# Kernel optimization log

Hardware: AMD Instinct MI355X
Metric: run time of the kernel (lower is better)

Reference implementation:

```python
import jax, jax.numpy as jnp
import numpy as np

B, T, D = 8, 1024, 768
H, DH = 12, 64
E, K, DFF = 16, 2, 3072
EPS = 1e-5


def _ln(x, w, b):
    m = x.mean(-1, keepdims=True)
    v = ((x - m) ** 2).mean(-1, keepdims=True)
    return (x - m) * jax.lax.rsqrt(v + EPS) * w + b


def setup_inputs() -> dict:
    key = jax.random.key(0)
    ks = jax.random.split(key, 12)
    s = 0.02
    return {
        "x": jax.random.normal(ks[0], (B, T, D), jnp.float32),
        "ln1_w": jnp.ones((D,), jnp.float32),
        "ln1_b": jnp.zeros((D,), jnp.float32),
        "qkv_w": jax.random.normal(ks[1], (D, 3 * D), jnp.float32) * s,
        "qkv_b": jnp.zeros((3 * D,), jnp.float32),
        "proj_w": jax.random.normal(ks[2], (D, D), jnp.float32) * s,
        "proj_b": jnp.zeros((D,), jnp.float32),
        "ln2_w": jnp.ones((D,), jnp.float32),
        "ln2_b": jnp.zeros((D,), jnp.float32),
        "router_w": jax.random.normal(ks[3], (D, E), jnp.float32) * s,
        "w1": jax.random.normal(ks[4], (E, D, DFF), jnp.float32) * s,
        "b1": jnp.zeros((E, DFF), jnp.float32),
        "w2": jax.random.normal(ks[5], (E, DFF, D), jnp.float32) * s,
        "b2": jnp.zeros((E, D), jnp.float32),
    }


def _block(x, ln1_w, ln1_b, qkv_w, qkv_b, proj_w, proj_b,
           ln2_w, ln2_b, router_w, w1, b1, w2, b2):
    # --- attention ---
    h = _ln(x, ln1_w, ln1_b)
    qkv = h @ qkv_w + qkv_b                      # [B,T,3D]
    q, k, v = jnp.split(qkv, 3, axis=-1)
    q = q.reshape(B, T, H, DH).transpose(0, 2, 1, 3)
    k = k.reshape(B, T, H, DH).transpose(0, 2, 1, 3)
    v = v.reshape(B, T, H, DH).transpose(0, 2, 1, 3)
    scores = jnp.einsum("bhqd,bhkd->bhqk", q, k) / np.sqrt(DH)
    causal = jnp.tril(jnp.ones((T, T), bool))
    scores = jnp.where(causal, scores, -jnp.inf)
    attn = jax.nn.softmax(scores, axis=-1)
    y = jnp.einsum("bhqk,bhkd->bhqd", attn, v)
    y = y.transpose(0, 2, 1, 3).reshape(B, T, D)
    x = x + y @ proj_w + proj_b                  # residual 1

    # --- MoE FFN (dense all-experts, gated combine) ---
    z = _ln(x, ln2_w, ln2_b)                     # [B,T,D]
    probs = jax.nn.softmax(z @ router_w, axis=-1)  # [B,T,E]
    top_p, ix = jax.lax.top_k(probs, K)
    gate = (jax.nn.one_hot(ix, E, dtype=probs.dtype) * top_p[..., None]).sum(-2)  # [B,T,E]
    gate_e = jnp.moveaxis(gate, -1, 0)           # [E,B,T]

    def body(acc, ew):
        g, W1, B1, W2, B2 = ew
        out = jax.nn.gelu(z @ W1 + B1, approximate=False) @ W2 + B2
        return acc + g[..., None] * out, None

    yff, _ = jax.lax.scan(body, jnp.zeros_like(z), (gate_e, w1, b1, w2, b2))
    # MoELayer returns z + yff; Block adds x again (faithful double residual)
    return x + z + yff


def reference(x, ln1_w, ln1_b, qkv_w, qkv_b, proj_w, proj_b,
              ln2_w, ln2_b, router_w, w1, b1, w2, b2):
    return _block(x, ln1_w, ln1_b, qkv_w, qkv_b, proj_w, proj_b,
                  ln2_w, ln2_b, router_w, w1, b1, w2, b2)
```

## Files before the change

kernel.cpp:

```cpp
#include <hip/hip_runtime.h>
#include <math.h>

#define D_MODEL 768
#define T_SEQ   1024
#define B_BATCH 8
#define NTOK    8192
#define H_HEADS 12
#define DHEAD   64
#define NEXP    16
#define DFF     3072
#define NPAIR   16384
#define MAXT128 144
#define MAXT256 80

typedef unsigned short u16;
typedef unsigned int   u32;

typedef __attribute__((ext_vector_type(8))) short bf16x8;
typedef __attribute__((ext_vector_type(4))) float f32x4;
typedef __attribute__((ext_vector_type(4))) u32   u32x4;

__device__ __forceinline__ float bf2f(u16 u) { return __uint_as_float(((u32)u) << 16); }
__device__ __forceinline__ u16 f2bf(float f) {
    u32 u = __float_as_uint(f);
    return (u16)((u + 0x7FFFu + ((u >> 16) & 1u)) >> 16);
}

__device__ __forceinline__ float fast_gelu(float v) {
    float u2 = -1.5957691216f * v * (1.0f + 0.044715f * v * v);
    return v / (1.0f + __expf(u2));
}

__device__ __forceinline__ void gload16(const void* g, void* l) {
    __builtin_amdgcn_global_load_lds((const __attribute__((address_space(1))) void*)g,
                                     (__attribute__((address_space(3))) void*)l, 16, 0, 0);
}

__global__ __launch_bounds__(256) void ln_kernel(const float* __restrict__ x,
                                                 const float* __restrict__ w,
                                                 const float* __restrict__ b,
                                                 u16* __restrict__ out_bf,
                                                 float* __restrict__ out_f) {
    const int row = blockIdx.x;
    const int tid = threadIdx.x;
    const float* xr = x + (size_t)row * D_MODEL;
    float v0 = xr[tid], v1 = xr[tid + 256], v2 = xr[tid + 512];
    float s = v0 + v1 + v2;
    float s2 = v0 * v0 + v1 * v1 + v2 * v2;
#pragma unroll
    for (int o = 32; o > 0; o >>= 1) { s += __shfl_down(s, o); s2 += __shfl_down(s2, o); }
    __shared__ float red[8];
    __shared__ float stats[2];
    const int wid = tid >> 6;
    if ((tid & 63) == 0) { red[wid] = s; red[4 + wid] = s2; }
    __syncthreads();
    if (tid == 0) {
        float ts = red[0] + red[1] + red[2] + red[3];
        float ts2 = red[4] + red[5] + red[6] + red[7];
        float mean = ts * (1.0f / D_MODEL);
        float var = ts2 * (1.0f / D_MODEL) - mean * mean;
        stats[0] = mean;
        stats[1] = rsqrtf(var + 1e-5f);
    }
    __syncthreads();
    const float mean = stats[0], rstd = stats[1];
    u16* orow = out_bf + (size_t)row * D_MODEL;
    float r0 = (v0 - mean) * rstd * w[tid]       + b[tid];
    float r1 = (v1 - mean) * rstd * w[tid + 256] + b[tid + 256];
    float r2 = (v2 - mean) * rstd * w[tid + 512] + b[tid + 512];
    orow[tid] = f2bf(r0); orow[tid + 256] = f2bf(r1); orow[tid + 512] = f2bf(r2);
    if (out_f) {
        float* frow = out_f + (size_t)row * D_MODEL;
        frow[tid] = r0; frow[tid + 256] = r1; frow[tid + 512] = r2;
    }
}

__global__ __launch_bounds__(256) void transpose_cvt(const float* __restrict__ src,
                                                     u16* __restrict__ dst,
                                                     int R, int C) {
    const size_t plane = (size_t)R * C;
    src += (size_t)blockIdx.z * plane;
    dst += (size_t)blockIdx.z * plane;
    __shared__ __align__(16) u16 tile[64][72];
    const int t = threadIdx.x;
    const int r0 = blockIdx.y * 64, c0 = blockIdx.x * 64;
    {
        const int lr = t >> 2, lc = (t & 3) * 16;
        const float* sp = src + (size_t)(r0 + lr) * C + c0 + lc;
        u16 tmp[16];
#pragma unroll
        for (int j = 0; j < 4; ++j) {
            f32x4 f = *(const f32x4*)(sp + j * 4);
            tmp[j * 4 + 0] = f2bf(f[0]); tmp[j * 4 + 1] = f2bf(f[1]);
            tmp[j * 4 + 2] = f2bf(f[2]); tmp[j * 4 + 3] = f2bf(f[3]);
        }
        *(u32x4*)&tile[lr][lc]     = *(const u32x4*)&tmp[0];
        *(u32x4*)&tile[lr][lc + 8] = *(const u32x4*)&tmp[8];
    }
    __syncthreads();
    {
        const int ln = t >> 2, lk0 = (t & 3) * 16;
        u16 o[16];
#pragma unroll
        for (int j = 0; j < 16; ++j) o[j] = tile[lk0 + j][ln];
        u16* d = dst + (size_t)(c0 + ln) * R + r0 + lk0;
        *(u32x4*)&d[0] = *(const u32x4*)&o[0];
        *(u32x4*)&d[8] = *(const u32x4*)&o[8];
    }
}

template <int MODE>
__global__ __launch_bounds__(512, 4) void gemm256(
    const u16* __restrict__ A, const u16* __restrict__ Bt,
    const float* __restrict__ bias, void* __restrict__ Cout,
    const float* __restrict__ resid,
    const int* __restrict__ bucket_tok, const int* __restrict__ offsets,
    const int* __restrict__ counts, const int* __restrict__ desc_e,
    const int* __restrict__ desc_r, const int* __restrict__ tile_cnt,
    int K, int N)
{
    const u32 nwg  = gridDim.x * gridDim.y;
    const u32 orig = blockIdx.x + gridDim.x * blockIdx.y;
    const u32 flat = (nwg & 7u) ? orig : ((orig & 7u) * (nwg >> 3) + (orig >> 3));
    const int bx = (int)(flat % gridDim.x);
    const int by = (int)(flat / gridDim.x);

    int e = 0, r0 = 0, off = 0, ne = 0, row0 = 0;
    const int col0 = bx * 128;
    if constexpr (MODE >= 2) {
        if (by >= *tile_cnt) return;
        e = desc_e[by];
        r0 = desc_r[by];
        off = offsets[e];
        ne = counts[e];
    } else {
        row0 = by * 256;
    }
    if constexpr (MODE == 2) Bt += (size_t)e * D_MODEL * DFF;
    if constexpr (MODE == 3) Bt += (size_t)e * DFF * D_MODEL;

    __shared__ __align__(16) u16 AsBs[256 * 64 + 128 * 64];
    u16* As = AsBs;
    u16* Bs = AsBs + 256 * 64;

    const int tid = threadIdx.x;
    const int lane = tid & 63;
    const int w = tid >> 6;
    const int wm = w >> 1, wn = w & 1;
    const int fr = lane & 15, fg = lane >> 4;

    const int koff = ((((tid & 7) * 16) ^ (((tid >> 3) & 7) << 4)) >> 1);

    u32 aoff[4];
#pragma unroll
    for (int i = 0; i < 4; ++i) {
        const int r = i * 64 + (tid >> 3);
        u32 row;
        if constexpr (MODE == 2) {
            int rb = r0 + r;
            row = (u32)bucket_tok[off + (rb < ne ? rb : 0)];
        } else if constexpr (MODE == 3) {
            int rb = r0 + r;
            row = (u32)(off + (rb < ne ? rb : (ne - 1)));
        } else {
            row = (u32)(row0 + r);
        }
        aoff[i] = row * (u32)K + (u32)koff;
    }
    u32 boff[2];
#pragma unroll
    for (int i = 0; i < 2; ++i) {
        const int n = i * 64 + (tid >> 3);
        boff[i] = (u32)(col0 + n) * (u32)K + (u32)koff;
    }

    f32x4 acc[4][4] = {};

    for (int k0 = 0; k0 < K; k0 += 64) {
        __syncthreads();
#pragma unroll
        for (int i = 0; i < 4; ++i)
            gload16(A + aoff[i] + k0, &As[(i * 512 + w * 64) * 8]);
#pragma unroll
        for (int i = 0; i < 2; ++i)
            gload16(Bt + boff[i] + k0, &Bs[(i * 512 + w * 64) * 8]);
        __syncthreads();
#pragma unroll
        for (int kk = 0; kk < 2; ++kk) {
            const int sw = ((kk * 64 + fg * 16) ^ ((fr & 7) << 4)) >> 1;
            bf16x8 a[4], b[4];
#pragma unroll
            for (int mi = 0; mi < 4; ++mi)
                a[mi] = *(const bf16x8*)&As[(wm * 64 + mi * 16 + fr) * 64 + sw];
#pragma unroll
            for (int ni = 0; ni < 4; ++ni)
                b[ni] = *(const bf16x8*)&Bs[(wn * 64 + ni * 16 + fr) * 64 + sw];
#pragma unroll
            for (int mi = 0; mi < 4; ++mi)
#pragma unroll
                for (int ni = 0; ni < 4; ++ni)
                    acc[mi][ni] = __builtin_amdgcn_mfma_f32_16x16x32_bf16(a[mi], b[ni], acc[mi][ni], 0, 0, 0);
        }
    }

    __syncthreads();
    float* slab = (float*)AsBs + w * 1088;
    const int er = lane >> 2;
    const int ec = (lane & 3) * 16;
    const int colb = col0 + wn * 64 + ec;

#pragma unroll
    for (int mi = 0; mi < 4; ++mi) {
#pragma unroll
        for (int ni = 0; ni < 4; ++ni)
#pragma unroll
            for (int i = 0; i < 4; ++i)
                slab[(fg * 4 + i) * 68 + ni * 16 + fr] = acc[mi][ni][i];
        __syncthreads();
        f32x4 v[4];
#pragma unroll
        for (int q = 0; q < 4; ++q) v[q] = *(const f32x4*)&slab[er * 68 + ec + q * 4];
        const int lrow = wm * 64 + mi * 16 + er;

        if constexpr (MODE == 0) {
            u16 o[16];
#pragma unroll
            for (int q = 0; q < 4; ++q) {
                f32x4 b4 = *(const f32x4*)&bias[colb + q * 4];
#pragma unroll
                for (int j = 0; j < 4; ++j) o[q * 4 + j] = f2bf(v[q][j] + b4[j]);
            }
            u16* cp = (u16*)Cout + (size_t)(row0 + lrow) * N + colb;
            *(u32x4*)cp       = *(const u32x4*)&o[0];
            *(u32x4*)(cp + 8) = *(const u32x4*)&o[8];
        } else if constexpr (MODE == 1) {
            float* cp = (float*)Cout + (size_t)(row0 + lrow) * N + colb;
            const float* rp = resid + (size_t)(row0 + lrow) * N + colb;
#pragma unroll
            for (int q = 0; q < 4; ++q) {
                f32x4 b4 = *(const f32x4*)&bias[colb + q * 4];
                f32x4 r4 = *(const f32x4*)(rp + q * 4);
                f32x4 o4;
#pragma unroll
                for (int j = 0; j < 4; ++j) o4[j] = v[q][j] + b4[j] + r4[j];
                *(f32x4*)(cp + q * 4) = o4;
            }
        } else if constexpr (MODE == 2) {
            const int rb = r0 + lrow;
            if (rb < ne) {
                u16 o[16];
#pragma unroll
                for (int q = 0; q < 4; ++q) {
                    f32x4 b4 = *(const f32x4*)&bias[(size_t)e * DFF + colb + q * 4];
#pragma unroll
                    for (int j = 0; j < 4; ++j) o[q * 4 + j] = f2bf(fast_gelu(v[q][j] + b4[j]));
                }
                u16* cp = (u16*)Cout + (size_t)(off + rb) * N + colb;
                *(u32x4*)cp       = *(const u32x4*)&o[0];
                *(u32x4*)(cp + 8) = *(const u32x4*)&o[8];
            }
        } else {
            const int rb = r0 + lrow;
            if (rb < ne) {
                float* cp = (float*)Cout + (size_t)(off + rb) * N + colb;
#pragma unroll
                for (int q = 0; q < 4; ++q) {
                    f32x4 b4 = *(const f32x4*)&bias[(size_t)e * D_MODEL + colb + q * 4];
                    f32x4 o4;
#pragma unroll
                    for (int j = 0; j < 4; ++j) o4[j] = v[q][j] + b4[j];
                    *(f32x4*)(cp + q * 4) = o4;
                }
            }
        }
        if (mi < 3) __syncthreads();
    }
}

template <int MODE>
__global__ __launch_bounds__(256) void gemm128f(
    const u16* __restrict__ A, const float* __restrict__ Bf,
    const float* __restrict__ bias, void* __restrict__ Cout,
    const float* __restrict__ resid,
    const int* __restrict__ bucket_tok, const int* __restrict__ offsets,
    const int* __restrict__ counts, const int* __restrict__ desc_e,
    const int* __restrict__ desc_r, const int* __restrict__ tile_cnt,
    int K, int N)
{
    int e = 0, r0 = 0, off = 0, ne = 0, row0 = 0;
    const int col0 = blockIdx.x * 128;
    if constexpr (MODE >= 2) {
        if ((int)blockIdx.y >= *tile_cnt) return;
        e = desc_e[blockIdx.y]; r0 = desc_r[blockIdx.y];
        off = offsets[e]; ne = counts[e];
    } else row0 = blockIdx.y * 128;
    if constexpr (MODE == 2) Bf += (size_t)e * D_MODEL * DFF;
    if constexpr (MODE == 3) Bf += (size_t)e * DFF * D_MODEL;

    __shared__ __align__(16) u16 AsL[128 * 32];
    __shared__ __align__(16) u16 BsL[128 * 32];

    const int tid = threadIdx.x;
    const int lane = tid & 63;
    const int w = tid >> 6;
    const int wr = (w >> 1) * 64, wc = (w & 1) * 64;
    const int fr = lane & 15, fg = lane >> 4;
    const int lrow = lane >> 2, lk = (lane & 3) * 8;

    const u16* ag[2];
#pragma unroll
    for (int i = 0; i < 2; ++i) {
        int r = i * 64 + w * 16 + lrow;
        size_t srow;
        if constexpr (MODE == 2) {
            int rb = r0 + r;
            int tok = bucket_tok[off + (rb < ne ? rb : 0)];
            srow = (size_t)tok * K;
        } else if constexpr (MODE == 3) {
            int rb = r0 + r;
            int pp = off + (rb < ne ? rb : (ne - 1));
            srow = (size_t)pp * K;
        } else srow = (size_t)(row0 + r) * K;
        ag[i] = A + srow + lk;
    }

    f32x4 acc[4][4] = {};
    for (int k0 = 0; k0 < K; k0 += 32) {
        __syncthreads();
        gload16(ag[0] + k0, &AsL[0 * 2048 + w * 512]);
        gload16(ag[1] + k0, &AsL[1 * 2048 + w * 512]);
#pragma unroll
        for (int i = 0; i < 4; ++i) {
            int s = tid + 256 * i;
            int kk = s >> 5, n4 = (s & 31) * 4;
            f32x4 f = *(const f32x4*)(Bf + (size_t)(k0 + kk) * N + col0 + n4);
            BsL[(n4 + 0) * 32 + kk] = f2bf(f[0]);
            BsL[(n4 + 1) * 32 + kk] = f2bf(f[1]);
            BsL[(n4 + 2) * 32 + kk] = f2bf(f[2]);
            BsL[(n4 + 3) * 32 + kk] = f2bf(f[3]);
        }
        __syncthreads();
        bf16x8 a[4], b[4];
#pragma unroll
        for (int mi = 0; mi < 4; ++mi)
            a[mi] = *(const bf16x8*)&AsL[(wr + mi * 16 + fr) * 32 + fg * 8];
#pragma unroll
        for (int ni = 0; ni < 4; ++ni)
            b[ni] = *(const bf16x8*)&BsL[(wc + ni * 16 + fr) * 32 + fg * 8];
#pragma unroll
        for (int mi = 0; mi < 4; ++mi)
#pragma unroll
            for (int ni = 0; ni < 4; ++ni)
                acc[mi][ni] = __builtin_amdgcn_mfma_f32_16x16x32_bf16(a[mi], b[ni], acc[mi][ni], 0, 0, 0);
    }
#pragma unroll
    for (int mi = 0; mi < 4; ++mi) {
#pragma unroll
        for (int ni = 0; ni < 4; ++ni) {
            const int lr = wr + mi * 16 + fg * 4;
            const int col = col0 + wc + ni * 16 + fr;
#pragma unroll
            for (int i = 0; i < 4; ++i) {
                float v = acc[mi][ni][i];
                if constexpr (MODE == 0) {
                    int grow = row0 + lr + i;
                    ((u16*)Cout)[(size_t)grow * N + col] = f2bf(v + bias[col]);
                } else if constexpr (MODE == 1) {
                    int grow = row0 + lr + i;
                    size_t idx = (size_t)grow * N + col;
                    ((float*)Cout)[idx] = resid[idx] + v + bias[col];
                } else if constexpr (MODE == 2) {
                    int rb = r0 + lr + i;
                    if (rb < ne) {
                        float vb = v + bias[(size_t)e * DFF + col];
                        ((u16*)Cout)[(size_t)(off + rb) * N + col] = f2bf(fast_gelu(vb));
                    }
                } else {
                    int rb = r0 + lr + i;
                    if (rb < ne) {
                        ((float*)Cout)[(size_t)(off + rb) * N + col] = v + bias[(size_t)e * D_MODEL + col];
                    }
                }
            }
        }
    }
}

__global__ __launch_bounds__(256) void attn_mfma(const u16* __restrict__ qkv,
                                                 u16* __restrict__ y) {
    const int bh = blockIdx.x;
    const int b = bh / H_HEADS, h = bh % H_HEADS;
    const int qt = gridDim.y - 1 - blockIdx.y;
    const int tid = threadIdx.x, lane = tid & 63, w = tid >> 6;
    const int fr = lane & 15, fg = lane >> 4;

    __shared__ __align__(16) u16 Ks[64][72];
    __shared__ __align__(16) u16 Vt[64][72];
    __shared__ __align__(16) u16 Ps[4][32][72];

    const int tb = b * T_SEQ + qt * 128;
    const int wrow = w * 32;

    bf16x8 aq[2][2];
#pragma unroll
    for (int rg = 0; rg < 2; ++rg) {
        const u16* qp = qkv + (size_t)(tb + wrow + rg * 16 + fr) * (3 * D_MODEL) + h * DHEAD + fg * 8;
        aq[rg][0] = *(const bf16x8*)qp;
        aq[rg][1] = *(const bf16x8*)(qp + 32);
    }
    f32x4 accO[2][4] = {};
    float m_[2][4], l_[2][4];
#pragma unroll
    for (int rg = 0; rg < 2; ++rg)
#pragma unroll
        for (int i = 0; i < 4; ++i) { m_[rg][i] = -1e30f; l_[rg][i] = 0.0f; }

    const int ktmax = 2 * qt + 1;
    for (int kt = 0; kt <= ktmax; ++kt) {
        __syncthreads();
        {
            const int krow = tid >> 2, c16 = (tid & 3) * 16;
            const u16* kp = qkv + (size_t)(b * T_SEQ + kt * 64 + krow) * (3 * D_MODEL)
                          + D_MODEL + h * DHEAD + c16;
            *(u32x4*)&Ks[krow][c16]     = *(const u32x4*)kp;
            *(u32x4*)&Ks[krow][c16 + 8] = *(const u32x4*)(kp + 8);
            const u16* vp = kp + D_MODEL;
            u16 vv[16];
            *(u32x4*)&vv[0] = *(const u32x4*)vp;
            *(u32x4*)&vv[8] = *(const u32x4*)(vp + 8);
#pragma unroll
            for (int j = 0; j < 16; ++j) Vt[c16 + j][krow] = vv[j];
        }
        __syncthreads();

        if (kt * 64 > qt * 128 + wrow + 31) continue;

#pragma unroll
        for (int rg = 0; rg < 2; ++rg) {
            f32x4 s4[4] = {};
#pragma unroll
            for (int kk = 0; kk < 2; ++kk) {
#pragma unroll
                for (int ni = 0; ni < 4; ++ni) {
                    bf16x8 bk = *(const bf16x8*)&Ks[ni * 16 + fr][kk * 32 + fg * 8];
                    s4[ni] = __builtin_amdgcn_mfma_f32_16x16x32_bf16(aq[rg][kk], bk, s4[ni], 0, 0, 0);
                }
            }
            float p[4][4];
#pragma unroll
            for (int i = 0; i < 4; ++i) {
                const int grow = qt * 128 + wrow + rg * 16 + fg * 4 + i;
                float rmax = -1e30f;
#pragma unroll
                for (int ni = 0; ni < 4; ++ni) {
                    float v = s4[ni][i] * 0.125f;
                    if (kt * 64 + ni * 16 + fr > grow) v = -1e30f;
                    p[ni][i] = v;
                    rmax = fmaxf(rmax, v);
                }
#pragma unroll
                for (int msk = 1; msk < 16; msk <<= 1) rmax = fmaxf(rmax, __shfl_xor(rmax, msk));
                const float mn = fmaxf(m_[rg][i], rmax);
                float sum = 0.0f;
#pragma unroll
                for (int ni = 0; ni < 4; ++ni) {
                    float ev = __expf(p[ni][i] - mn);
                    p[ni][i] = ev;
                    sum += ev;
                }
#pragma unroll
                for (int msk = 1; msk < 16; msk <<= 1) sum += __shfl_xor(sum, msk);
                const float sc = __expf(m_[rg][i] - mn);
                l_[rg][i] = l_[rg][i] * sc + sum;
                m_[rg][i] = mn;
#pragma unroll
                for (int ni = 0; ni < 4; ++ni) accO[rg][ni][i] *= sc;
#pragma unroll
                for (int ni = 0; ni < 4; ++ni)
                    Ps[w][rg * 16 + fg * 4 + i][ni * 16 + fr] = f2bf(p[ni][i]);
            }
        }

#pragma unroll
        for (int rg = 0; rg < 2; ++rg) {
#pragma unroll
            for (int kk = 0; kk < 2; ++kk) {
                bf16x8 ap = *(const bf16x8*)&Ps[w][rg * 16 + fr][kk * 32 + fg * 8];
#pragma unroll
                for (int ni = 0; ni < 4; ++ni) {
                    bf16x8 bv = *(const bf16x8*)&Vt[ni * 16 + fr][kk * 32 + fg * 8];
                    accO[rg][ni] = __builtin_amdgcn_mfma_f32_16x16x32_bf16(ap, bv, accO[rg][ni], 0, 0, 0);
                }
            }
        }
    }

#pragma unroll
    for (int rg = 0; rg < 2; ++rg) {
#pragma unroll
        for (int i = 0; i < 4; ++i) {
            const float inv = 1.0f / l_[rg][i];
            u16* yp = y + (size_t)(tb + wrow + rg * 16 + fg * 4 + i) * D_MODEL + h * DHEAD;
#pragma unroll
            for (int ni = 0; ni < 4; ++ni) yp[ni * 16 + fr] = f2bf(accO[rg][ni][i] * inv);
        }
    }
}

__global__ __launch_bounds__(64) void router_kernel(const float* __restrict__ z,
                                                    const float* __restrict__ rw,
                                                    float* __restrict__ gates,
                                                    int* __restrict__ eidx) {
    const int t = blockIdx.x;
    const int lane = threadIdx.x;
    const int e = lane & 15, part = lane >> 4;
    const float* zr = z + (size_t)t * D_MODEL;
    float acc = 0.0f;
    for (int d = part * 192; d < part * 192 + 192; ++d)
        acc += zr[d] * rw[d * NEXP + e];
    acc += __shfl_down(acc, 32);
    acc += __shfl_down(acc, 16);
    const float lg = acc;
    float logit[NEXP];
#pragma unroll
    for (int ee = 0; ee < NEXP; ++ee) logit[ee] = __shfl(lg, ee);
    if (lane == 0) {
        float m1 = -1e30f, m2 = -1e30f; int i1 = 0, i2 = 0;
#pragma unroll
        for (int ee = 0; ee < NEXP; ++ee) {
            float v = logit[ee];
            if (v > m1) { m2 = m1; i2 = i1; m1 = v; i1 = ee; }
            else if (v > m2) { m2 = v; i2 = ee; }
        }
        float den = 0.0f;
#pragma unroll
        for (int ee = 0; ee < NEXP; ++ee) den += __expf(logit[ee] - m1);
        const float inv = 1.0f / den;
        gates[2 * t] = inv;
        gates[2 * t + 1] = __expf(m2 - m1) * inv;
        eidx[2 * t] = i1;
        eidx[2 * t + 1] = i2;
    }
}

__global__ __launch_bounds__(256) void count_kernel(const int* __restrict__ eidx, int* counts) {
    int i = blockIdx.x * 256 + threadIdx.x;
    if (i < NPAIR) atomicAdd(&counts[eidx[i]], 1);
}

__global__ void offsets_kernel(const int* __restrict__ counts, int* offsets, int* cursor,
                               int* desc_e, int* desc_r, int* tile_cnt, int step) {
    if (threadIdx.x == 0 && blockIdx.x == 0) {
        int off = 0, nt = 0;
        for (int e = 0; e < NEXP; ++e) {
            offsets[e] = off;
            cursor[e] = off;
            int c = counts[e];
            for (int r = 0; r < c; r += step) { desc_e[nt] = e; desc_r[nt] = r; ++nt; }
            off += c;
        }
        *tile_cnt = nt;
    }
}

__global__ __launch_bounds__(256) void scatter_kernel(const int* __restrict__ eidx, int* cursor,
                                                      int* __restrict__ btok, int* __restrict__ ppos) {
    int i = blockIdx.x * 256 + threadIdx.x;
    if (i < NPAIR) {
        int pos = atomicAdd(&cursor[eidx[i]], 1);
        btok[pos] = i >> 1;
        ppos[i] = pos;
    }
}

__global__ __launch_bounds__(256) void final_kernel(const float* __restrict__ x1,
                                                    const float* __restrict__ zf,
                                                    const float* __restrict__ moe_o,
                                                    const float* __restrict__ gates,
                                                    const int* __restrict__ ppos,
                                                    float* __restrict__ out) {
    const int t = blockIdx.x;
    const int d = blockIdx.y * 256 + threadIdx.x;
    const size_t idx = (size_t)t * D_MODEL + d;
    const float g0 = gates[2 * t], g1 = gates[2 * t + 1];
    const int p0 = ppos[2 * t], p1 = ppos[2 * t + 1];
    out[idx] = x1[idx] + zf[idx] + g0 * moe_o[(size_t)p0 * D_MODEL + d]
                                 + g1 * moe_o[(size_t)p1 * D_MODEL + d];
}

extern "C" void kernel_launch(void* const* d_in, const int* in_sizes, int n_in,
                              void* d_out, int out_size, void* d_ws, size_t ws_size,
                              hipStream_t stream) {
    const float* x        = (const float*)d_in[0];
    const float* ln1_w    = (const float*)d_in[1];
    const float* ln1_b    = (const float*)d_in[2];
    const float* qkv_w    = (const float*)d_in[3];
    const float* qkv_b    = (const float*)d_in[4];
    const float* proj_w   = (const float*)d_in[5];
    const float* proj_b   = (const float*)d_in[6];
    const float* ln2_w    = (const float*)d_in[7];
    const float* ln2_b    = (const float*)d_in[8];
    const float* router_w = (const float*)d_in[9];
    const float* w1       = (const float*)d_in[10];
    const float* b1       = (const float*)d_in[11];
    const float* w2       = (const float*)d_in[12];
    const float* b2       = (const float*)d_in[13];
    float* out = (float*)d_out;

    char* ws = (char*)d_ws;
    size_t off = 0;
    auto alloc = [&](size_t bytes) -> void* {
        void* p = ws + off;
        off += (bytes + 255) & ~(size_t)255;
        return p;
    };
    u16*  h_bf   = (u16*)alloc((size_t)NTOK * D_MODEL * 2);
    u16*  qkv_bf = (u16*)alloc((size_t)NTOK * 3 * D_MODEL * 2);
    u16*  y_bf   = h_bf;
    float* x1    = (float*)alloc((size_t)NTOK * D_MODEL * 4);
    u16*  z_bf   = (u16*)alloc((size_t)NTOK * D_MODEL * 2);
    float* z_f   = (float*)alloc((size_t)NTOK * D_MODEL * 4);
    u16*  act    = (u16*)alloc((size_t)NPAIR * DFF * 2);
    float* moe_o = (float*)alloc((size_t)NPAIR * D_MODEL * 4);
    float* gates = (float*)alloc((size_t)NTOK * 2 * 4);
    int*  eidx   = (int*)alloc((size_t)NTOK * 2 * 4);
    int*  ppos   = (int*)alloc((size_t)NTOK * 2 * 4);
    int*  btok   = (int*)alloc((size_t)NPAIR * 4);
    int*  counts = (int*)alloc(NEXP * 4);
    int*  offs   = (int*)alloc(NEXP * 4);
    int*  cursor = (int*)alloc(NEXP * 4);
    int*  desc_e = (int*)alloc(MAXT128 * 4);
    int*  desc_r = (int*)alloc(MAXT128 * 4);
    int*  tcnt   = (int*)alloc(4);
    u16* qkvT  = (u16*)alloc((size_t)(3 * D_MODEL) * D_MODEL * 2);
    u16* projT = (u16*)alloc((size_t)D_MODEL * D_MODEL * 2);
    u16* w1t   = (u16*)alloc((size_t)NEXP * DFF * D_MODEL * 2);
    u16* w2t   = (u16*)alloc((size_t)NEXP * D_MODEL * DFF * 2);
    const bool useT = (off <= ws_size);
    (void)in_sizes; (void)n_in; (void)out_size;

    hipMemsetAsync(counts, 0, NEXP * 4, stream);

    if (useT) {
        transpose_cvt<<<dim3(3 * D_MODEL / 64, D_MODEL / 64, 1), 256, 0, stream>>>(qkv_w, qkvT, D_MODEL, 3 * D_MODEL);
        transpose_cvt<<<dim3(D_MODEL / 64, D_MODEL / 64, 1), 256, 0, stream>>>(proj_w, projT, D_MODEL, D_MODEL);
        transpose_cvt<<<dim3(DFF / 64, D_MODEL / 64, NEXP), 256, 0, stream>>>(w1, w1t, D_MODEL, DFF);
        transpose_cvt<<<dim3(D_MODEL / 64, DFF / 64, NEXP), 256, 0, stream>>>(w2, w2t, DFF, D_MODEL);
    }

    ln_kernel<<<NTOK, 256, 0, stream>>>(x, ln1_w, ln1_b, h_bf, nullptr);
    if (useT)
        gemm256<0><<<dim3(18, 32), 512, 0, stream>>>(h_bf, qkvT, qkv_b, qkv_bf, nullptr,
            nullptr, nullptr, nullptr, nullptr, nullptr, nullptr, D_MODEL, 3 * D_MODEL);
    else
        gemm128f<0><<<dim3(18, 64), 256, 0, stream>>>(h_bf, qkv_w, qkv_b, qkv_bf, nullptr,
            nullptr, nullptr, nullptr, nullptr, nullptr, nullptr, D_MODEL, 3 * D_MODEL);

    attn_mfma<<<dim3(B_BATCH * H_HEADS, T_SEQ / 128), 256, 0, stream>>>(qkv_bf, y_bf);

    if (useT)
        gemm256<1><<<dim3(6, 32), 512, 0, stream>>>(y_bf, projT, proj_b, x1, x,
            nullptr, nullptr, nullptr, nullptr, nullptr, nullptr, D_MODEL, D_MODEL);
    else
        gemm128f<1><<<dim3(6, 64), 256, 0, stream>>>(y_bf, proj_w, proj_b, x1, x,
            nullptr, nullptr, nullptr, nullptr, nullptr, nullptr, D_MODEL, D_MODEL);

    ln_kernel<<<NTOK, 256, 0, stream>>>(x1, ln2_w, ln2_b, z_bf, z_f);
    router_kernel<<<NTOK, 64, 0, stream>>>(z_f, router_w, gates, eidx);
    count_kernel<<<NPAIR / 256, 256, 0, stream>>>(eidx, counts);
    offsets_kernel<<<1, 64, 0, stream>>>(counts, offs, cursor, desc_e, desc_r, tcnt,
                                         useT ? 256 : 128);
    scatter_kernel<<<NPAIR / 256, 256, 0, stream>>>(eidx, cursor, btok, ppos);

    if (useT) {
        gemm256<2><<<dim3(DFF / 128, MAXT256), 512, 0, stream>>>(z_bf, w1t, b1, act, nullptr,
            btok, offs, counts, desc_e, desc_r, tcnt, D_MODEL, DFF);
        gemm256<3><<<dim3(D_MODEL / 128, MAXT256), 512, 0, stream>>>(act, w2t, b2, moe_o, nullptr,
            btok, offs, counts, desc_e, desc_r, tcnt, DFF, D_MODEL);
    } else {
        gemm128f<2><<<dim3(DFF / 128, MAXT128), 256, 0, stream>>>(z_bf, w1, b1, act, nullptr,
            btok, offs, counts, desc_e, desc_r, tcnt, D_MODEL, DFF);
        gemm128f<3><<<dim3(D_MODEL / 128, MAXT128), 256, 0, stream>>>(act, w2, b2, moe_o, nullptr,
            btok, offs, counts, desc_e, desc_r, tcnt, DFF, D_MODEL);
    }

    final_kernel<<<dim3(NTOK, 3), 256, 0, stream>>>(x1, z_f, moe_o, gates, ppos, out);
}
```

Measured before the change: 665.2 us.

## Add double-buffered 256x256-tile GEMM for QKV and MoE expert matmuls

Adds a new GEMM kernel with 256x256 output tiles, with each wave computing a 128x64 sub-tile, and double-buffered LDS so the next K-slice's global loads overlap the current MFMA work. It is used for the QKV projection and both MoE expert GEMMs. The projection GEMM keeps the old single-buffered 256x128 kernel, now specialized to residual mode only. The larger tiles raise data reuse per byte loaded, but use 128 KB of LDS and twice the accumulator registers, which lowers occupancy. They also give fewer workgroups per launch, so the small-N MoE down-projection gets only 3 column tiles.

```diff
diff --git a/kernel.cpp b/kernel.cpp
--- a/kernel.cpp
+++ b/kernel.cpp
@@ -110,10 +110,9 @@
 }
 
 template <int MODE>
-__global__ __launch_bounds__(512, 4) void gemm256(
+__global__ __launch_bounds__(512, 2) void gemm2ph(
     const u16* __restrict__ A, const u16* __restrict__ Bt,
     const float* __restrict__ bias, void* __restrict__ Cout,
-    const float* __restrict__ resid,
     const int* __restrict__ bucket_tok, const int* __restrict__ offsets,
     const int* __restrict__ counts, const int* __restrict__ desc_e,
     const int* __restrict__ desc_r, const int* __restrict__ tile_cnt,
@@ -126,7 +125,7 @@
     const int by = (int)(flat / gridDim.x);
 
     int e = 0, r0 = 0, off = 0, ne = 0, row0 = 0;
-    const int col0 = bx * 128;
+    const int col0 = bx * 256;
     if constexpr (MODE >= 2) {
         if (by >= *tile_cnt) return;
         e = desc_e[by];
@@ -139,19 +138,18 @@
     if constexpr (MODE == 2) Bt += (size_t)e * D_MODEL * DFF;
     if constexpr (MODE == 3) Bt += (size_t)e * DFF * D_MODEL;
 
-    __shared__ __align__(16) u16 AsBs[256 * 64 + 128 * 64];
-    u16* As = AsBs;
-    u16* Bs = AsBs + 256 * 64;
+    __shared__ __align__(16) u16 As[2][256 * 64];
+    __shared__ __align__(16) u16 Bs[2][256 * 64];
 
     const int tid = threadIdx.x;
     const int lane = tid & 63;
     const int w = tid >> 6;
-    const int wm = w >> 1, wn = w & 1;
+    const int wm = w >> 2, wn = w & 3;
     const int fr = lane & 15, fg = lane >> 4;
 
     const int koff = ((((tid & 7) * 16) ^ (((tid >> 3) & 7) << 4)) >> 1);
 
-    u32 aoff[4];
+    u32 aoff[4], boff[4];
 #pragma unroll
     for (int i = 0; i < 4; ++i) {
         const int r = i * 64 + (tid >> 3);
@@ -166,51 +164,58 @@
             row = (u32)(row0 + r);
         }
         aoff[i] = row * (u32)K + (u32)koff;
-    }
-    u32 boff[2];
-#pragma unroll
-    for (int i = 0; i < 2; ++i) {
-        const int n = i * 64 + (tid >> 3);
-        boff[i] = (u32)(col0 + n) * (u32)K + (u32)koff;
-    }
-
-    f32x4 acc[4][4] = {};
-
-    for (int k0 = 0; k0 < K; k0 += 64) {
-        __syncthreads();
-#pragma unroll
-        for (int i = 0; i < 4; ++i)
-            gload16(A + aoff[i] + k0, &As[(i * 512 + w * 64) * 8]);
-#pragma unroll
-        for (int i = 0; i < 2; ++i)
-            gload16(Bt + boff[i] + k0, &Bs[(i * 512 + w * 64) * 8]);
-        __syncthreads();
+        boff[i] = (u32)(col0 + r) * (u32)K + (u32)koff;
+    }
+
+    f32x4 acc[8][4] = {};
+    const int nt = K >> 6;
+
+#pragma unroll
+    for (int i = 0; i < 4; ++i) gload16(A + aoff[i],  &As[0][(i * 512 + w * 64) * 8]);
+#pragma unroll
+    for (int i = 0; i < 4; ++i) gload16(Bt + boff[i], &Bs[0][(i * 512 + w * 64) * 8]);
+    __syncthreads();
+
+    int cur = 0;
+    for (int t = 0; t < nt; ++t) {
+        if (t + 1 < nt) {
+            const int k0n = (t + 1) * 64;
+            const int nxt = cur ^ 1;
+#pragma unroll
+            for (int i = 0; i < 4; ++i) gload16(A + aoff[i] + k0n,  &As[nxt][(i * 512 + w * 64) * 8]);
+#pragma unroll
+            for (int i = 0; i < 4; ++i) gload16(Bt + boff[i] + k0n, &Bs[nxt][(i * 512 + w * 64) * 8]);
+        }
 #pragma unroll
         for (int kk = 0; kk < 2; ++kk) {
             const int sw = ((kk * 64 + fg * 16) ^ ((fr & 7) << 4)) >> 1;
-            bf16x8 a[4], b[4];
-#pragma unroll
-            for (int mi = 0; mi < 4; ++mi)
-                a[mi] = *(const bf16x8*)&As[(wm * 64 + mi * 16 + fr) * 64 + sw];
+            bf16x8 a[8], b[4];
+#pragma unroll
+            for (int mi = 0; mi < 8; ++mi)
+                a[mi] = *(const bf16x8*)&As[cur][(wm * 128 + mi * 16 + fr) * 64 + sw];
 #pragma unroll
             for (int ni = 0; ni < 4; ++ni)
-                b[ni] = *(const bf16x8*)&Bs[(wn * 64 + ni * 16 + fr) * 64 + sw];
-#pragma unroll
-            for (int mi = 0; mi < 4; ++mi)
+                b[ni] = *(const bf16x8*)&Bs[cur][(wn * 64 + ni * 16 + fr) * 64 + sw];
+#pragma unroll
+            for (int mi = 0; mi < 8; ++mi)
 #pragma unroll
                 for (int ni = 0; ni < 4; ++ni)
                     acc[mi][ni] = __builtin_amdgcn_mfma_f32_16x16x32_bf16(a[mi], b[ni], acc[mi][ni], 0, 0, 0);
         }
+        if (t + 1 < nt) {
+            __syncthreads();
+            cur ^= 1;
+        }
     }
 
     __syncthreads();
-    float* slab = (float*)AsBs + w * 1088;
+    float* slab = (float*)&As[0][0] + w * 1088;
     const int er = lane >> 2;
     const int ec = (lane & 3) * 16;
     const int colb = col0 + wn * 64 + ec;
 
 #pragma unroll
-    for (int mi = 0; mi < 4; ++mi) {
+    for (int mi = 0; mi < 8; ++mi) {
 #pragma unroll
         for (int ni = 0; ni < 4; ++ni)
 #pragma unroll
@@ -220,7 +225,7 @@
         f32x4 v[4];
 #pragma unroll
         for (int q = 0; q < 4; ++q) v[q] = *(const f32x4*)&slab[er * 68 + ec + q * 4];
-        const int lrow = wm * 64 + mi * 16 + er;
+        const int lrow = wm * 128 + mi * 16 + er;
 
         if constexpr (MODE == 0) {
             u16 o[16];
@@ -233,18 +238,6 @@
             u16* cp = (u16*)Cout + (size_t)(row0 + lrow) * N + colb;
             *(u32x4*)cp       = *(const u32x4*)&o[0];
             *(u32x4*)(cp + 8) = *(const u32x4*)&o[8];
-        } else if constexpr (MODE == 1) {
-            float* cp = (float*)Cout + (size_t)(row0 + lrow) * N + colb;
-            const float* rp = resid + (size_t)(row0 + lrow) * N + colb;
-#pragma unroll
-            for (int q = 0; q < 4; ++q) {
-                f32x4 b4 = *(const f32x4*)&bias[colb + q * 4];
-                f32x4 r4 = *(const f32x4*)(rp + q * 4);
-                f32x4 o4;
-#pragma unroll
-                for (int j = 0; j < 4; ++j) o4[j] = v[q][j] + b4[j] + r4[j];
-                *(f32x4*)(cp + q * 4) = o4;
-            }
         } else if constexpr (MODE == 2) {
             const int rb = r0 + lrow;
             if (rb < ne) {
@@ -272,6 +265,106 @@
                     *(f32x4*)(cp + q * 4) = o4;
                 }
             }
+        }
+        if (mi < 7) __syncthreads();
+    }
+}
+
+template <int MODE>
+__global__ __launch_bounds__(512, 4) void gemm256(
+    const u16* __restrict__ A, const u16* __restrict__ Bt,
+    const float* __restrict__ bias, void* __restrict__ Cout,
+    const float* __restrict__ resid,
+    int K, int N)
+{
+    const u32 nwg  = gridDim.x * gridDim.y;
+    const u32 orig = blockIdx.x + gridDim.x * blockIdx.y;
+    const u32 flat = (nwg & 7u) ? orig : ((orig & 7u) * (nwg >> 3) + (orig >> 3));
+    const int bx = (int)(flat % gridDim.x);
+    const int by = (int)(flat / gridDim.x);
+
+    const int col0 = bx * 128;
+    const int row0 = by * 256;
+
+    __shared__ __align__(16) u16 AsBs[256 * 64 + 128 * 64];
+    u16* As = AsBs;
+    u16* Bs = AsBs + 256 * 64;
+
+    const int tid = threadIdx.x;
+    const int lane = tid & 63;
+    const int w = tid >> 6;
+    const int wm = w >> 1, wn = w & 1;
+    const int fr = lane & 15, fg = lane >> 4;
+
+    const int koff = ((((tid & 7) * 16) ^ (((tid >> 3) & 7) << 4)) >> 1);
+
+    u32 aoff[4];
+#pragma unroll
+    for (int i = 0; i < 4; ++i)
+        aoff[i] = (u32)(row0 + i * 64 + (tid >> 3)) * (u32)K + (u32)koff;
+    u32 boff[2];
+#pragma unroll
+    for (int i = 0; i < 2; ++i)
+        boff[i] = (u32)(col0 + i * 64 + (tid >> 3)) * (u32)K + (u32)koff;
+
+    f32x4 acc[4][4] = {};
+
+    for (int k0 = 0; k0 < K; k0 += 64) {
+        __syncthreads();
+#pragma unroll
+        for (int i = 0; i < 4; ++i)
+            gload16(A + aoff[i] + k0, &As[(i * 512 + w * 64) * 8]);
+#pragma unroll
+        for (int i = 0; i < 2; ++i)
+            gload16(Bt + boff[i] + k0, &Bs[(i * 512 + w * 64) * 8]);
+        __syncthreads();
+#pragma unroll
+        for (int kk = 0; kk < 2; ++kk) {
+            const int sw = ((kk * 64 + fg * 16) ^ ((fr & 7) << 4)) >> 1;
+            bf16x8 a[4], b[4];
+#pragma unroll
+            for (int mi = 0; mi < 4; ++mi)
+                a[mi] = *(const bf16x8*)&As[(wm * 64 + mi * 16 + fr) * 64 + sw];
+#pragma unroll
+            for (int ni = 0; ni < 4; ++ni)
+                b[ni] = *(const bf16x8*)&Bs[(wn * 64 + ni * 16 + fr) * 64 + sw];
+#pragma unroll
+            for (int mi = 0; mi < 4; ++mi)
+#pragma unroll
+                for (int ni = 0; ni < 4; ++ni)
+                    acc[mi][ni] = __builtin_amdgcn_mfma_f32_16x16x32_bf16(a[mi], b[ni], acc[mi][ni], 0, 0, 0);
+        }
+    }
+
+    __syncthreads();
+    float* slab = (float*)AsBs + w * 1088;
+    const int er = lane >> 2;
+    const int ec = (lane & 3) * 16;
+    const int colb = col0 + wn * 64 + ec;
+
+#pragma unroll
+    for (int mi = 0; mi < 4; ++mi) {
+#pragma unroll
+        for (int ni = 0; ni < 4; ++ni)
+#pragma unroll
+            for (int i = 0; i < 4; ++i)
+                slab[(fg * 4 + i) * 68 + ni * 16 + fr] = acc[mi][ni][i];
+        __syncthreads();
+        f32x4 v[4];
+#pragma unroll
+        for (int q = 0; q < 4; ++q) v[q] = *(const f32x4*)&slab[er * 68 + ec + q * 4];
+        const int lrow = wm * 64 + mi * 16 + er;
+
+        float* cp = (float*)Cout + (size_t)(row0 + lrow) * N + colb;
+        const float* rp = resid + (size_t)(row0 + lrow) * N + colb;
+#pragma unroll
+        for (int q = 0; q < 4; ++q) {
+            f32x4 b4 = *(const f32x4*)&bias[colb + q * 4];
+            f32x4 r4 = *(const f32x4*)(rp + q * 4);
+            f32x4 o4;
+#pragma unroll
+            for (int j = 0; j < 4; ++j) o4[j] = v[q][j] + b4[j] + r4[j];
+            *(f32x4*)(cp + q * 4) = o4;
         }
         if (mi < 3) __syncthreads();
     }
@@ -650,7 +743,7 @@
 
     ln_kernel<<<NTOK, 256, 0, stream>>>(x, ln1_w, ln1_b, h_bf, nullptr);
     if (useT)
-        gemm256<0><<<dim3(18, 32), 512, 0, stream>>>(h_bf, qkvT, qkv_b, qkv_bf, nullptr,
+        gemm2ph<0><<<dim3(9, 32), 512, 0, stream>>>(h_bf, qkvT, qkv_b, qkv_bf,
             nullptr, nullptr, nullptr, nullptr, nullptr, nullptr, D_MODEL, 3 * D_MODEL);
     else
         gemm128f<0><<<dim3(18, 64), 256, 0, stream>>>(h_bf, qkv_w, qkv_b, qkv_bf, nullptr,
@@ -660,7 +753,7 @@
 
     if (useT)
         gemm256<1><<<dim3(6, 32), 512, 0, stream>>>(y_bf, projT, proj_b, x1, x,
-            nullptr, nullptr, nullptr, nullptr, nullptr, nullptr, D_MODEL, D_MODEL);
+            D_MODEL, D_MODEL);
     else
         gemm128f<1><<<dim3(6, 64), 256, 0, stream>>>(y_bf, proj_w, proj_b, x1, x,
             nullptr, nullptr, nullptr, nullptr, nullptr, nullptr, D_MODEL, D_MODEL);
@@ -673,9 +766,9 @@
     scatter_kernel<<<NPAIR / 256, 256, 0, stream>>>(eidx, cursor, btok, ppos);
 
     if (useT) {
-        gemm256<2><<<dim3(DFF / 128, MAXT256), 512, 0, stream>>>(z_bf, w1t, b1, act, nullptr,
+        gemm2ph<2><<<dim3(DFF / 256, MAXT256), 512, 0, stream>>>(z_bf, w1t, b1, act,
             btok, offs, counts, desc_e, desc_r, tcnt, D_MODEL, DFF);
-        gemm256<3><<<dim3(D_MODEL / 128, MAXT256), 512, 0, stream>>>(act, w2t, b2, moe_o, nullptr,
+        gemm2ph<3><<<dim3(D_MODEL / 256, MAXT256), 512, 0, stream>>>(act, w2t, b2, moe_o,
             btok, offs, counts, desc_e, desc_r, tcnt, DFF, D_MODEL);
     } else {
         gemm128f<2><<<dim3(DFF / 128, MAXT128), 256, 0, stream>>>(z_bf, w1, b1, act, nullptr,
```

After: 659.1 us (median of 2 runs). About the same (-0.9%).
